# Kernel optimization log

Measured on AMD Instinct MI355X. Metric: run time of the kernel, lower is better.

Reference implementation:

```python
import jax, jax.numpy as jnp
import numpy as np

G = 64  # fixed grid size hardcoded in the torch module

def setup_inputs() -> dict:
    key = jax.random.key(0)
    ks = jax.random.split(key, 12)
    N, H = 500000, 256
    s = lambda fan_in: 1.0 / np.sqrt(fan_in)
    return {
        "positions": jax.random.normal(ks[0], (N, 3), jnp.float32) * 2.0,
        "grid_points": jax.random.normal(ks[1], (G, 3), jnp.float32) * 2.0,
        "W1": jax.random.normal(ks[2], (3, 64), jnp.float32) * s(3),
        "b1": jnp.zeros((64,), jnp.float32),
        "W2": jax.random.normal(ks[3], (64, 128), jnp.float32) * s(64),
        "b2": jnp.zeros((128,), jnp.float32),
        "W3": jax.random.normal(ks[4], (128, H), jnp.float32) * s(128),
        "b3": jnp.zeros((H,), jnp.float32),
        "Wn1": jax.random.normal(ks[5], (H, H), jnp.float32) * s(H),
        "bn1": jnp.zeros((H,), jnp.float32),
        "Wn2": jax.random.normal(ks[6], (H, H), jnp.float32) * s(H),
        "bn2": jnp.zeros((H,), jnp.float32),
        "Wh1": jax.random.normal(ks[7], (4, H, 128), jnp.float32) * s(H),
        "bh1": jnp.zeros((4, 128), jnp.float32),
        "Wh2": jax.random.normal(ks[8], (4, 128, 1), jnp.float32) * s(128),
        "bh2": jnp.zeros((4, 1), jnp.float32),
    }

def reference(positions, grid_points, W1, b1, W2, b2, W3, b3,
              Wn1, bn1, Wn2, bn2, Wh1, bh1, Wh2, bh2):
    # crystal_encoder: per-atom MLP 3 -> 64 -> 128 -> 256 over ALL N atoms
    h = jax.nn.relu(positions @ W1 + b1)
    h = jax.nn.relu(h @ W2 + b2)
    feat = h @ W3 + b3                                   # [N, H]

    # _map_crystal_to_grid: only the first min(N, 64) atoms are mapped.
    pos64 = positions[:G]                                # [64, 3]
    d2 = jnp.sum((pos64[:, None, :] - grid_points[None, :, :]) ** 2, axis=-1)
    idx = jnp.argmin(d2, axis=-1)                        # [64] nearest grid point per atom
    winner = jnp.full((G,), -1, jnp.int32).at[idx].max(jnp.arange(G, dtype=jnp.int32))
    grid_feats = jnp.where(winner[:, None] >= 0,
                           feat[jnp.clip(winner, 0)], 0.0)  # [64, H]

    # TetrahedralAGINetwork (per-node MLP, channels-first output convention)
    x = grid_feats[None]                                 # [1, 64, H]
    y = jax.nn.relu(x @ Wn1 + bn1) @ Wn2 + bn2           # [1, 64, H]
    agg = jnp.mean(jnp.swapaxes(y, 1, 2), axis=-1)       # mean over nodes -> [1, H]

    # 4 property heads, batched: [4, 1, 1] -> [4] (order: band_gap,
    # elastic_modulus, thermal_conductivity, dielectric_constant)
    h1 = jax.nn.relu(jnp.einsum('bc,kcd->kbd', agg, Wh1) + bh1[:, None, :])
    props = jnp.einsum('kbd,kdo->kbo', h1, Wh2) + bh2[:, None, :]
    return props.reshape(4)
```

## Files before the change

kernel.cpp:

```cpp
#include <hip/hip_runtime.h>


__device__ __forceinline__ void async_cp16(const float* g, float* l) {
    __builtin_amdgcn_global_load_lds(
        (const __attribute__((address_space(1))) void*)g,
        (__attribute__((address_space(3))) void*)l, 16, 0, 0);
}
__device__ __forceinline__ void stage_contig(const float* g, float* l, int nfloats, int tid) {
    const int lane = tid & 63, wv = tid >> 6;
    const int ninst = nfloats >> 8;
    for (int i = wv; i < ninst; i += 4)
        async_cp16(g + i*256 + lane*4, l + i*256);
}
__device__ __forceinline__ void stage_slice32(const float* g, float* l, int ld, int j0, int nrows, int tid) {
    const int lane = tid & 63, wv = tid >> 6;
    const int r = lane >> 3, c4 = (lane & 7) << 2;
    const int ninst = nrows >> 3;
    for (int i = wv; i < ninst; i += 4)
        async_cp16(g + (i*8 + r)*ld + j0 + c4, l + i*256);
}

#define A_SMEM_BYTES (32768*4)

__global__ __launch_bounds__(256) void a_gf(
    const float* __restrict__ positions, const float* __restrict__ grid_pts,
    const float* __restrict__ W1, const float* __restrict__ b1,
    const float* __restrict__ W2, const float* __restrict__ b2,
    const float* __restrict__ W3, const float* __restrict__ b3,
    float* __restrict__ gf_ws)
{
    extern __shared__ float w3s[];
    __shared__ float pos_s[192], grid_s[192], w1_s[192], b1_s[64];
    __shared__ int   idx_s[64], win_s[8];
    __shared__ __align__(16) float h1s[8*64];
    __shared__ __align__(16) float h2s[8*128];

    const int tid = threadIdx.x;
    const int bg  = blockIdx.x;

    stage_contig(W3, w3s, 32768, tid);
    if (tid < 192) { pos_s[tid] = positions[tid]; grid_s[tid] = grid_pts[tid]; w1_s[tid] = W1[tid]; }
    if (tid >= 192) b1_s[tid - 192] = b1[tid - 192];
    const float bb2 = b2[tid & 127];
    const float bb3 = b3[tid];
    __syncthreads();

    if (tid < 64) {
        const float px = pos_s[tid*3], py = pos_s[tid*3+1], pz = pos_s[tid*3+2];
        float best = 3.4e38f; int bi = 0;
        for (int g = 0; g < 64; ++g) {
            const float dx = px - grid_s[g*3];
            const float dy = py - grid_s[g*3+1];
            const float dz = pz - grid_s[g*3+2];
            const float d2 = dx*dx + dy*dy + dz*dz;
            if (d2 < best) { best = d2; bi = g; }
        }
        idx_s[tid] = bi;
    }
    __syncthreads();
    if (tid < 8) {
        const int g = bg*8 + tid;
        int m = -1;
        for (int i = 0; i < 64; ++i) if (idx_s[i] == g) m = i;
        win_s[tid] = m;
    }
    __syncthreads();

    #pragma unroll
    for (int u = 0; u < 2; ++u) {
        const int e  = tid + u*256;
        const int lr = e >> 6, k = e & 63;
        int r = win_s[lr]; if (r < 0) r = 0;
        const float acc = b1_s[k] + pos_s[r*3]*w1_s[k] + pos_s[r*3+1]*w1_s[64+k]
                                  + pos_s[r*3+2]*w1_s[128+k];
        h1s[lr*64 + k] = fmaxf(acc, 0.f);
    }
    __syncthreads();

    {
        const int d = tid & 127, t0 = tid >> 7;
        float acc[4];
        #pragma unroll
        for (int m = 0; m < 4; ++m) acc[m] = bb2;
        for (int kc = 0; kc < 64; kc += 16) {
            float w[16];
            #pragma unroll
            for (int u = 0; u < 16; ++u) w[u] = W2[(kc+u)*128 + d];
            #pragma unroll
            for (int u = 0; u < 16; u += 4) {
                #pragma unroll
                for (int m = 0; m < 4; ++m) {
                    const float4 h4 = *(const float4*)&h1s[(t0 + 2*m)*64 + kc + u];
                    acc[m] += h4.x*w[u] + h4.y*w[u+1] + h4.z*w[u+2] + h4.w*w[u+3];
                }
            }
        }
        #pragma unroll
        for (int m = 0; m < 4; ++m)
            h2s[(t0 + 2*m)*128 + d] = fmaxf(acc[m], 0.f);
    }
    __syncthreads();

    {
        const int j = tid;
        float ag[8];
        #pragma unroll
        for (int t = 0; t < 8; ++t) ag[t] = 0.f;
        for (int dc = 0; dc < 128; dc += 16) {
            float w[16];
            #pragma unroll
            for (int u = 0; u < 16; ++u) w[u] = w3s[(dc+u)*256 + j];
            #pragma unroll
            for (int u = 0; u < 16; u += 4) {
                #pragma unroll
                for (int t = 0; t < 8; ++t) {
                    const float4 h4 = *(const float4*)&h2s[t*128 + dc + u];
                    ag[t] += h4.x*w[u] + h4.y*w[u+1] + h4.z*w[u+2] + h4.w*w[u+3];
                }
            }
        }
        #pragma unroll
        for (int t = 0; t < 8; ++t)
            gf_ws[(bg*8 + t)*256 + j] = (win_s[t] >= 0) ? (ag[t] + bb3) : 0.f;
    }
}

__global__ __launch_bounds__(256) void k2_tpart(
    const float* __restrict__ Wn1, const float* __restrict__ bn1,
    const float* __restrict__ gf_ws, float* __restrict__ tpart_ws)
{
    __shared__ __align__(16) float wn1_s[256*32];
    __shared__ __align__(16) float gf_s[8*256];
    __shared__ float r_s[256];

    const int tid = threadIdx.x;
    const int bg  = blockIdx.x >> 3;
    const int j0  = (blockIdx.x & 7) * 32;
    stage_slice32(Wn1, wn1_s, 256, j0, 256, tid);
    stage_contig(gf_ws + bg*8*256, gf_s, 8*256, tid);

    const int jl = tid & 31, t = tid >> 5;
    const float bb = bn1[j0 + jl];
    __syncthreads();

    float acc = bb;
    for (int cc = 0; cc < 256; cc += 32) {
        float w[32];
        #pragma unroll
        for (int u = 0; u < 32; ++u) w[u] = wn1_s[(cc+u)*32 + jl];
        #pragma unroll
        for (int u = 0; u < 32; u += 4) {
            const float4 g4 = *(const float4*)&gf_s[t*256 + cc + u];
            acc += g4.x*w[u] + g4.y*w[u+1] + g4.z*w[u+2] + g4.w*w[u+3];
        }
    }
    r_s[tid] = fmaxf(acc, 0.f);
    __syncthreads();
    if (t == 0) {
        float ps = 0.f;
        #pragma unroll
        for (int tt = 0; tt < 8; ++tt) ps += r_s[tt*32 + jl];
        tpart_ws[bg*256 + j0 + jl] = ps;
    }
}

__global__ __launch_bounds__(256) void k3_agg(
    const float* __restrict__ Wn2, const float* __restrict__ bn2,
    const float* __restrict__ tpart_ws, float* __restrict__ agg_ws)
{
    __shared__ __align__(16) float wn2_s[256*32];
    __shared__ __align__(16) float tp_s[8*256];
    __shared__ __align__(16) float tbars[256];

    const int tid = threadIdx.x;
    const int c0  = blockIdx.x * 32;
    stage_slice32(Wn2, wn2_s, 256, c0, 256, tid);
    stage_contig(tpart_ws, tp_s, 8*256, tid);

    const float bb = (tid < 32) ? bn2[c0 + tid] : 0.f;
    __syncthreads();

    {
        float tb = 0.f;
        #pragma unroll
        for (int q = 0; q < 8; ++q) tb += tp_s[q*256 + tid];
        tbars[tid] = tb * (1.f/64.f);
    }
    __syncthreads();

    if (tid < 32) {
        float acc = bb;
        for (int jc = 0; jc < 256; jc += 32) {
            float w[32];
            #pragma unroll
            for (int u = 0; u < 32; ++u) w[u] = wn2_s[(jc+u)*32 + tid];
            #pragma unroll
            for (int u = 0; u < 32; u += 4) {
                const float4 t4 = *(const float4*)&tbars[jc + u];
                acc += t4.x*w[u] + t4.y*w[u+1] + t4.z*w[u+2] + t4.w*w[u+3];
            }
        }
        agg_ws[c0 + tid] = acc;
    }
}

#define D_SMEM_BYTES (32768*4)

__global__ __launch_bounds__(256) void d_heads(
    const float* __restrict__ Wh1, const float* __restrict__ bh1,
    const float* __restrict__ Wh2, const float* __restrict__ bh2,
    const float* __restrict__ agg_ws, float* __restrict__ out)
{
    extern __shared__ float wh1s[];
    __shared__ __align__(16) float agg_s[256];
    __shared__ __align__(16) float h1h_s[128];
    __shared__ __align__(16) float wh2_s[128];

    const int tid = threadIdx.x;
    const int k   = blockIdx.x;

    stage_contig(Wh1 + k*32768, wh1s, 32768, tid);
    stage_contig(agg_ws, agg_s, 256, tid);
    const float bbh1 = (tid < 128) ? bh1[k*128 + tid] : 0.f;
    if (tid < 128) wh2_s[tid] = Wh2[k*128 + tid];
    const float bbh2 = bh2[k];
    __syncthreads();

    if (tid < 128) {
        const int d = tid;
        float acc = bbh1;
        for (int cc = 0; cc < 256; cc += 16) {
            float wa[16];
            #pragma unroll
            for (int u = 0; u < 16; ++u) wa[u] = wh1s[(cc+u)*128 + d];
            #pragma unroll
            for (int u = 0; u < 16; u += 4) {
                const float4 a4 = *(const float4*)&agg_s[cc + u];
                acc += a4.x*wa[u] + a4.y*wa[u+1] + a4.z*wa[u+2] + a4.w*wa[u+3];
            }
        }
        h1h_s[d] = fmaxf(acc, 0.f);
    }
    __syncthreads();
    if (tid == 0) {
        float acc = bbh2;
        for (int d = 0; d < 128; ++d) acc += h1h_s[d] * wh2_s[d];
        out[k] = acc;
    }
}

extern "C" void kernel_launch(void* const* d_in, const int* in_sizes, int n_in,
                              void* d_out, int out_size, void* d_ws, size_t ws_size,
                              hipStream_t stream) {
    const float* positions = (const float*)d_in[0];
    const float* grid      = (const float*)d_in[1];
    const float* W1  = (const float*)d_in[2];
    const float* b1  = (const float*)d_in[3];
    const float* W2  = (const float*)d_in[4];
    const float* b2  = (const float*)d_in[5];
    const float* W3  = (const float*)d_in[6];
    const float* b3  = (const float*)d_in[7];
    const float* Wn1 = (const float*)d_in[8];
    const float* bn1 = (const float*)d_in[9];
    const float* Wn2 = (const float*)d_in[10];
    const float* bn2 = (const float*)d_in[11];
    const float* Wh1 = (const float*)d_in[12];
    const float* bh1 = (const float*)d_in[13];
    const float* Wh2 = (const float*)d_in[14];
    const float* bh2 = (const float*)d_in[15];
    float* out = (float*)d_out;

    char* ws = (char*)d_ws;
    float* gf_ws    = (float*)(ws + 0);
    float* tpart_ws = (float*)(ws + 65536);
    float* agg_ws   = (float*)(ws + 73728);

    (void)hipFuncSetAttribute((const void*)a_gf,
                              hipFuncAttributeMaxDynamicSharedMemorySize,
                              A_SMEM_BYTES);
    (void)hipFuncSetAttribute((const void*)d_heads,
                              hipFuncAttributeMaxDynamicSharedMemorySize,
                              D_SMEM_BYTES);

    hipLaunchKernelGGL(a_gf,     dim3(8),  dim3(256), A_SMEM_BYTES, stream,
                       positions, grid, W1, b1, W2, b2, W3, b3, gf_ws);
    hipLaunchKernelGGL(k2_tpart, dim3(64), dim3(256), 0, stream,
                       Wn1, bn1, gf_ws, tpart_ws);
    hipLaunchKernelGGL(k3_agg,   dim3(8),  dim3(256), 0, stream,
                       Wn2, bn2, tpart_ws, agg_ws);
    hipLaunchKernelGGL(d_heads,  dim3(4),  dim3(256), D_SMEM_BYTES, stream,
                       Wh1, bh1, Wh2, bh2, agg_ws, out);
}
```

Baseline: 111.5 us.

## Fuse Wn2 aggregation into heads kernel with double-buffered weight staging

Merges the k3_agg and d_heads kernels into one cd_head kernel, so each of the 4 blocks redundantly computes the full 256-wide aggregated vector from the Wn2 weights before running its property head. This removes one kernel launch and the agg workspace round trip. In exchange, each block loads all of Wn2 (256 KB) instead of an eighth of it, with only 4 blocks doing that work. Wn2 and then Wh1 are streamed through two LDS halves, so the next chunk's load overlaps compute on the current one.

```diff
diff --git a/kernel.cpp b/kernel.cpp
--- a/kernel.cpp
+++ b/kernel.cpp
@@ -164,88 +164,127 @@
     }
 }
 
-__global__ __launch_bounds__(256) void k3_agg(
+#define CD_SMEM_BYTES (32768*4)
+
+__global__ __launch_bounds__(256) void cd_head(
     const float* __restrict__ Wn2, const float* __restrict__ bn2,
-    const float* __restrict__ tpart_ws, float* __restrict__ agg_ws)
-{
-    __shared__ __align__(16) float wn2_s[256*32];
-    __shared__ __align__(16) float tp_s[8*256];
-    __shared__ __align__(16) float tbars[256];
-
-    const int tid = threadIdx.x;
-    const int c0  = blockIdx.x * 32;
-    stage_slice32(Wn2, wn2_s, 256, c0, 256, tid);
-    stage_contig(tpart_ws, tp_s, 8*256, tid);
-
-    const float bb = (tid < 32) ? bn2[c0 + tid] : 0.f;
-    __syncthreads();
-
-    {
-        float tb = 0.f;
-        #pragma unroll
-        for (int q = 0; q < 8; ++q) tb += tp_s[q*256 + tid];
-        tbars[tid] = tb * (1.f/64.f);
-    }
-    __syncthreads();
-
-    if (tid < 32) {
-        float acc = bb;
-        for (int jc = 0; jc < 256; jc += 32) {
-            float w[32];
-            #pragma unroll
-            for (int u = 0; u < 32; ++u) w[u] = wn2_s[(jc+u)*32 + tid];
-            #pragma unroll
-            for (int u = 0; u < 32; u += 4) {
-                const float4 t4 = *(const float4*)&tbars[jc + u];
-                acc += t4.x*w[u] + t4.y*w[u+1] + t4.z*w[u+2] + t4.w*w[u+3];
-            }
-        }
-        agg_ws[c0 + tid] = acc;
-    }
-}
-
-#define D_SMEM_BYTES (32768*4)
-
-__global__ __launch_bounds__(256) void d_heads(
     const float* __restrict__ Wh1, const float* __restrict__ bh1,
     const float* __restrict__ Wh2, const float* __restrict__ bh2,
-    const float* __restrict__ agg_ws, float* __restrict__ out)
+    const float* __restrict__ tpart_ws,
+    float* __restrict__ out)
 {
-    extern __shared__ float wh1s[];
+    extern __shared__ float sm[];
+    __shared__ __align__(16) float tp_s[2048];
+    __shared__ __align__(16) float tbar_s[256];
     __shared__ __align__(16) float agg_s[256];
     __shared__ __align__(16) float h1h_s[128];
     __shared__ __align__(16) float wh2_s[128];
 
+    float* bufA = sm;
+    float* bufB = sm + 16384;
+
     const int tid = threadIdx.x;
     const int k   = blockIdx.x;
 
-    stage_contig(Wh1 + k*32768, wh1s, 32768, tid);
-    stage_contig(agg_ws, agg_s, 256, tid);
-    const float bbh1 = (tid < 128) ? bh1[k*128 + tid] : 0.f;
+    stage_contig(tpart_ws, tp_s, 2048, tid);
+    stage_contig(Wn2,          bufA, 16384, tid);
+    stage_contig(Wn2 + 16384,  bufB, 16384, tid);
+    const float bbn2  = bn2[tid];
+    const float bbh1k = (tid < 128) ? bh1[k*128 + tid] : 0.f;
     if (tid < 128) wh2_s[tid] = Wh2[k*128 + tid];
-    const float bbh2 = bh2[k];
+    const float bbh2k = bh2[k];
+    __syncthreads();
+
+    {
+        float tb = 0.f;
+        #pragma unroll
+        for (int q = 0; q < 8; ++q) tb += tp_s[q*256 + tid];
+        tbar_s[tid] = tb * (1.f/64.f);
+    }
+    __syncthreads();
+
+    float acc = bbn2;
+    for (int jc = 0; jc < 64; jc += 32) {
+        float w[32];
+        #pragma unroll
+        for (int u = 0; u < 32; ++u) w[u] = bufA[(jc+u)*256 + tid];
+        #pragma unroll
+        for (int u = 0; u < 32; u += 4) {
+            const float4 t4 = *(const float4*)&tbar_s[jc + u];
+            acc += t4.x*w[u] + t4.y*w[u+1] + t4.z*w[u+2] + t4.w*w[u+3];
+        }
+    }
+    __syncthreads();
+    stage_contig(Wn2 + 32768, bufA, 16384, tid);
+    for (int jc = 64; jc < 128; jc += 32) {
+        float w[32];
+        #pragma unroll
+        for (int u = 0; u < 32; ++u) w[u] = bufB[(jc-64+u)*256 + tid];
+        #pragma unroll
+        for (int u = 0; u < 32; u += 4) {
+            const float4 t4 = *(const float4*)&tbar_s[jc + u];
+            acc += t4.x*w[u] + t4.y*w[u+1] + t4.z*w[u+2] + t4.w*w[u+3];
+        }
+    }
+    __syncthreads();
+    stage_contig(Wn2 + 49152, bufB, 16384, tid);
+    for (int jc = 128; jc < 192; jc += 32) {
+        float w[32];
+        #pragma unroll
+        for (int u = 0; u < 32; ++u) w[u] = bufA[(jc-128+u)*256 + tid];
+        #pragma unroll
+        for (int u = 0; u < 32; u += 4) {
+            const float4 t4 = *(const float4*)&tbar_s[jc + u];
+            acc += t4.x*w[u] + t4.y*w[u+1] + t4.z*w[u+2] + t4.w*w[u+3];
+        }
+    }
+    __syncthreads();
+    for (int jc = 192; jc < 256; jc += 32) {
+        float w[32];
+        #pragma unroll
+        for (int u = 0; u < 32; ++u) w[u] = bufB[(jc-192+u)*256 + tid];
+        #pragma unroll
+        for (int u = 0; u < 32; u += 4) {
+            const float4 t4 = *(const float4*)&tbar_s[jc + u];
+            acc += t4.x*w[u] + t4.y*w[u+1] + t4.z*w[u+2] + t4.w*w[u+3];
+        }
+    }
+    agg_s[tid] = acc;
+    __syncthreads();
+    stage_contig(Wh1 + k*32768,         bufA, 16384, tid);
+    stage_contig(Wh1 + k*32768 + 16384, bufB, 16384, tid);
     __syncthreads();
 
     if (tid < 128) {
         const int d = tid;
-        float acc = bbh1;
-        for (int cc = 0; cc < 256; cc += 16) {
+        float a = bbh1k;
+        for (int cc = 0; cc < 128; cc += 16) {
             float wa[16];
             #pragma unroll
-            for (int u = 0; u < 16; ++u) wa[u] = wh1s[(cc+u)*128 + d];
+            for (int u = 0; u < 16; ++u) wa[u] = bufA[(cc+u)*128 + d];
             #pragma unroll
             for (int u = 0; u < 16; u += 4) {
                 const float4 a4 = *(const float4*)&agg_s[cc + u];
-                acc += a4.x*wa[u] + a4.y*wa[u+1] + a4.z*wa[u+2] + a4.w*wa[u+3];
+                a += a4.x*wa[u] + a4.y*wa[u+1] + a4.z*wa[u+2] + a4.w*wa[u+3];
             }
         }
-        h1h_s[d] = fmaxf(acc, 0.f);
+        for (int cc = 128; cc < 256; cc += 16) {
+            float wa[16];
+            #pragma unroll
+            for (int u = 0; u < 16; ++u) wa[u] = bufB[(cc-128+u)*128 + d];
+            #pragma unroll
+            for (int u = 0; u < 16; u += 4) {
+                const float4 a4 = *(const float4*)&agg_s[cc + u];
+                a += a4.x*wa[u] + a4.y*wa[u+1] + a4.z*wa[u+2] + a4.w*wa[u+3];
+            }
+        }
+        h1h_s[d] = fmaxf(a, 0.f);
     }
     __syncthreads();
     if (tid == 0) {
-        float acc = bbh2;
-        for (int d = 0; d < 128; ++d) acc += h1h_s[d] * wh2_s[d];
-        out[k] = acc;
+        float a = bbh2k;
+        for (int d = 0; d < 128; ++d) a += h1h_s[d] * wh2_s[d];
+        out[k] = a;
     }
 }
 
@@ -273,21 +312,18 @@
     char* ws = (char*)d_ws;
     float* gf_ws    = (float*)(ws + 0);
     float* tpart_ws = (float*)(ws + 65536);
-    float* agg_ws   = (float*)(ws + 73728);
 
     (void)hipFuncSetAttribute((const void*)a_gf,
                               hipFuncAttributeMaxDynamicSharedMemorySize,
                               A_SMEM_BYTES);
-    (void)hipFuncSetAttribute((const void*)d_heads,
+    (void)hipFuncSetAttribute((const void*)cd_head,
                               hipFuncAttributeMaxDynamicSharedMemorySize,
-                              D_SMEM_BYTES);
+                              CD_SMEM_BYTES);
 
     hipLaunchKernelGGL(a_gf,     dim3(8),  dim3(256), A_SMEM_BYTES, stream,
                        positions, grid, W1, b1, W2, b2, W3, b3, gf_ws);
     hipLaunchKernelGGL(k2_tpart, dim3(64), dim3(256), 0, stream,
                        Wn1, bn1, gf_ws, tpart_ws);
-    hipLaunchKernelGGL(k3_agg,   dim3(8),  dim3(256), 0, stream,
-                       Wn2, bn2, tpart_ws, agg_ws);
-    hipLaunchKernelGGL(d_heads,  dim3(4),  dim3(256), D_SMEM_BYTES, stream,
-                       Wh1, bh1, Wh2, bh2, agg_ws, out);
-}
+    hipLaunchKernelGGL(cd_head,  dim3(4),  dim3(256), CD_SMEM_BYTES, stream,
+                       Wn2, bn2, Wh1, bh1, Wh2, bh2, tpart_ws, out);
+}
```

Result: no change. 110.1 us (-1.2%).
